# Kernel tuning notes

Hardware: AMD Instinct MI355X
Metric: run time of the kernel (lower is better)

Reference implementation:

```python
import jax, jax.numpy as jnp
import numpy as np

L = 2        # num_layers
D = 512      # d_model
H = 8        # heads
C = 512      # GAT per-head out channels (= d_model, concat=False -> mean over heads)
B, S, E = 4, 512, 4096
NEG = jnp.float32(-1e9)


def setup_inputs() -> dict:
    key = jax.random.key(0)
    ks = jax.random.split(key, 20)
    sc = 0.02  # weight init scale
    inp = {
        'x': jax.random.normal(ks[0], (B, S, D), jnp.float32),
        'Wq': jax.random.normal(ks[1], (L, D, D), jnp.float32) * sc,
        'bq': jnp.zeros((L, D), jnp.float32),
        'Wk': jax.random.normal(ks[2], (L, D, D), jnp.float32) * sc,
        'bk': jnp.zeros((L, D), jnp.float32),
        'Wv': jax.random.normal(ks[3], (L, D, D), jnp.float32) * sc,
        'bv': jnp.zeros((L, D), jnp.float32),
        'Wo': jax.random.normal(ks[4], (L, D, D), jnp.float32) * sc,
        'bo': jnp.zeros((L, D), jnp.float32),
        'gatW': jax.random.normal(ks[5], (L, D, H * C), jnp.float32) * sc,
        'att_src': jax.random.normal(ks[6], (L, H, C), jnp.float32) * sc,
        'att_dst': jax.random.normal(ks[7], (L, H, C), jnp.float32) * sc,
        'gat_bias': jnp.zeros((L, C), jnp.float32),
        'ln_g': jnp.ones((L, D), jnp.float32),
        'ln_b': jnp.zeros((L, D), jnp.float32),
        'input_len': jax.random.randint(ks[8], (B,), S // 2, S + 1, jnp.int32),
        'edges': jax.random.randint(ks[9], (B, 2, E), 0, S // 2, jnp.int32),
        'edge_num': jax.random.randint(ks[10], (B,), E // 2, E + 1, jnp.int32),
    }
    return inp


def layer_norm(x, g, b, eps=1e-5):
    m = x.mean(-1, keepdims=True)
    v = ((x - m) ** 2).mean(-1, keepdims=True)
    return (x - m) * jax.lax.rsqrt(v + eps) * g + b


def mha(x, pad_mask, Wq, bq, Wk, bk, Wv, bv, Wo, bo):
    # pad_mask: [B,S] True where padded (masked out)
    b, s, d = x.shape
    dh = d // H
    q = (x @ Wq + bq).reshape(b, s, H, dh)
    k = (x @ Wk + bk).reshape(b, s, H, dh)
    v = (x @ Wv + bv).reshape(b, s, H, dh)
    scores = jnp.einsum('bqhd,bkhd->bhqk', q, k) / jnp.float32(np.sqrt(dh))
    scores = jnp.where(pad_mask[:, None, None, :], NEG, scores)
    a = jax.nn.softmax(scores, axis=-1)
    o = jnp.einsum('bhqk,bkhd->bqhd', a, v).reshape(b, s, d)
    return o @ Wo + bo


def gat_single(x, edge_index, edge_mask, node_mask, W, a_src_w, a_dst_w, bias):
    # x: [S,D]; edge_index: [2,E]; GATConv(d_model,d_model,heads,concat=False)
    s = x.shape[0]
    h = (x @ W).reshape(s, H, C)
    a_src_n = (h * a_src_w).sum(-1)  # [S,H]
    a_dst_n = (h * a_dst_w).sum(-1)  # [S,H]
    # add self loops (PyG default) for valid nodes
    ar = jnp.arange(s, dtype=edge_index.dtype)
    src = jnp.concatenate([edge_index[0], ar])
    dst = jnp.concatenate([edge_index[1], ar])
    em = jnp.concatenate([edge_mask, node_mask])  # [E+S]
    alpha = jax.nn.leaky_relu(a_src_n[src] + a_dst_n[dst], 0.2)  # [E+S,H]
    alpha = jnp.where(em[:, None], alpha, NEG)
    amax = jax.ops.segment_max(alpha, dst, num_segments=s)  # [S,H]
    ex = jnp.exp(alpha - amax[dst]) * em[:, None].astype(alpha.dtype)
    denom = jax.ops.segment_sum(ex, dst, num_segments=s)
    coef = ex / (denom[dst] + 1e-16)
    msg = h[src] * coef[:, :, None]  # [E+S,H,C]
    out = jax.ops.segment_sum(msg, dst, num_segments=s)  # [S,H,C]
    return out.mean(axis=1) + bias  # concat=False -> mean over heads


def reference(x, Wq, bq, Wk, bk, Wv, bv, Wo, bo, gatW, att_src, att_dst,
              gat_bias, ln_g, ln_b, input_len, edges, edge_num):
    b, s, d = x.shape
    node_mask = jnp.arange(s)[None, :] < input_len[:, None]      # [B,S]
    edge_mask = jnp.arange(edges.shape[-1])[None, :] < edge_num[:, None]  # [B,E]
    pad_mask = ~node_mask
    out = x
    layer_outputs = []
    gat_b = jax.vmap(gat_single, in_axes=(0, 0, 0, 0, None, None, None, None))
    for i in range(L):
        out = mha(out, pad_mask, Wq[i], bq[i], Wk[i], bk[i], Wv[i], bv[i], Wo[i], bo[i])
        g = gat_b(out, edges, edge_mask, node_mask,
                  gatW[i], att_src[i], att_dst[i], gat_bias[i])
        y = jax.nn.relu(layer_norm(g, ln_g[i], ln_b[i])) + out
        out = jnp.where(node_mask[:, :, None], y, out)
        layer_outputs.append(out)
    return jnp.stack(layer_outputs)  # [L,B,S,D]
```

## Files before the change

kernel.cpp:

```cpp
#include <hip/hip_runtime.h>
#include <cstddef>

#define DMODEL 512
#define HEADS  8
#define DH     64
#define CCH    512
#define BATCH  4
#define SEQ    512
#define NEDGE  4096
#define NLAYER 2
#define HC     (HEADS*CCH)

typedef unsigned short bf16_t;
typedef __attribute__((ext_vector_type(8))) short short8;
typedef __attribute__((ext_vector_type(4))) float floatx4;

__device__ __forceinline__ bf16_t f2bf(float f){
  unsigned u = __float_as_uint(f);
  unsigned r = (u + 0x7FFFu + ((u>>16)&1u)) >> 16;
  return (bf16_t)r;
}
__device__ __forceinline__ float bf2f(bf16_t u){ return __uint_as_float(((unsigned)u)<<16); }

__global__ void k_zero(int* __restrict__ p, int n){
  int i = blockIdx.x*256 + threadIdx.x;
  if (i < n) p[i] = 0;
}

__global__ void k_f2b(const float* __restrict__ in, bf16_t* __restrict__ out, int n4){
  int i = blockIdx.x*256 + threadIdx.x;
  if (i < n4){
    float4 v = ((const float4*)in)[i];
    ushort4 o;
    o.x=f2bf(v.x); o.y=f2bf(v.y); o.z=f2bf(v.z); o.w=f2bf(v.w);
    ((ushort4*)out)[i]=o;
  }
}

struct WtJob { const float* W[10]; bf16_t* WT[10]; };
__global__ __launch_bounds__(256) void k_wt_all(WtJob j){
  __shared__ float T[32][65];
  int t = blockIdx.x, k0 = blockIdx.y*32;
  int wsel, n0, N;
  if (t < 64){ wsel = t>>3; n0 = (t&7)*64; N = 512; }
  else { int t2 = t-64; wsel = 8 + (t2>>6); n0 = (t2&63)*64; N = 4096; }
  const float* W = j.W[wsel];
  bf16_t* WT = j.WT[wsel];
  const int K = 512;
  int tid = threadIdx.x;
  int lk = tid>>3, ln = (tid&7)*8;
  const float* src = W + (size_t)(k0+lk)*N + n0 + ln;
  float4 v0 = *(const float4*)src;
  float4 v1 = *(const float4*)(src+4);
  T[lk][ln+0]=v0.x; T[lk][ln+1]=v0.y; T[lk][ln+2]=v0.z; T[lk][ln+3]=v0.w;
  T[lk][ln+4]=v1.x; T[lk][ln+5]=v1.y; T[lk][ln+6]=v1.z; T[lk][ln+7]=v1.w;
  __syncthreads();
  int wn = tid>>2, wk = (tid&3)*8;
  ushort4 o0, o1;
  o0.x=f2bf(T[wk+0][wn]); o0.y=f2bf(T[wk+1][wn]); o0.z=f2bf(T[wk+2][wn]); o0.w=f2bf(T[wk+3][wn]);
  o1.x=f2bf(T[wk+4][wn]); o1.y=f2bf(T[wk+5][wn]); o1.z=f2bf(T[wk+6][wn]); o1.w=f2bf(T[wk+7][wn]);
  bf16_t* dst = WT + (size_t)(n0+wn)*K + k0 + wk;
  *(ushort4*)dst = o0;
  *(ushort4*)(dst+4) = o1;
}

struct GemmB {
  const bf16_t* W; const float* bias; float* C; bf16_t* Cb;
  const float* att_s; const float* att_d; float* asrc; float* adst;
};
struct GemmB3 { GemmB g[3]; };

__global__ __launch_bounds__(256) void k_gemm_mfma(const bf16_t* __restrict__ A, GemmB3 p,
                                                   int N, int K){
  const GemmB& g = p.g[blockIdx.z];
  const bf16_t* Wt  = g.W;
  const float* bias = g.bias;
  float* C          = g.C;
  bf16_t* Cb        = g.Cb;
  __shared__ __align__(16) bf16_t As[2][64*72];
  __shared__ __align__(16) bf16_t Bs[2][64*72];
  int bm = blockIdx.x*64, bn = blockIdx.y*64;
  int tid = threadIdx.x;
  int wave = tid>>6, lane = tid&63;
  int wy = wave>>1, wx = wave&1;
  int quad = lane>>4, l16 = lane&15;
  floatx4 acc[2][2];
  #pragma unroll
  for (int i=0;i<2;i++)
    #pragma unroll
    for (int j=0;j<2;j++) acc[i][j] = (floatx4){0.f,0.f,0.f,0.f};
  int sr = tid>>2;
  int sc = (tid&3)<<4;
  const bf16_t* Aptr = A  + (size_t)(bm+sr)*K + sc;
  const bf16_t* Bptr = Wt + (size_t)(bn+sr)*K + sc;
  uint4 a0, a1, b0, b1;
  a0 = *(const uint4*)(Aptr);     a1 = *(const uint4*)(Aptr + 8);
  b0 = *(const uint4*)(Bptr);     b1 = *(const uint4*)(Bptr + 8);
  *(uint4*)(As[0] + sr*72 + sc)     = a0;
  *(uint4*)(As[0] + sr*72 + sc + 8) = a1;
  *(uint4*)(Bs[0] + sr*72 + sc)     = b0;
  *(uint4*)(Bs[0] + sr*72 + sc + 8) = b1;
  const int nk = K>>6;
  for (int k=0; k<nk; k++){
    __syncthreads();
    if (k+1 < nk){
      int ko = (k+1)<<6;
      a0 = *(const uint4*)(Aptr + ko);     a1 = *(const uint4*)(Aptr + ko + 8);
      b0 = *(const uint4*)(Bptr + ko);     b1 = *(const uint4*)(Bptr + ko + 8);
    }
    const bf16_t* Ab = As[k&1];
    const bf16_t* Bb = Bs[k&1];
    short8 af[2][2], bfr[2][2];
    #pragma unroll
    for (int i=0;i<2;i++){
      af[0][i] = *(const short8*)(Ab + (wy*32+i*16+l16)*72 + quad*8);
      af[1][i] = *(const short8*)(Ab + (wy*32+i*16+l16)*72 + 32 + quad*8);
    }
    #pragma unroll
    for (int j=0;j<2;j++){
      bfr[0][j] = *(const short8*)(Bb + (wx*32+j*16+l16)*72 + quad*8);
      bfr[1][j] = *(const short8*)(Bb + (wx*32+j*16+l16)*72 + 32 + quad*8);
    }
    #pragma unroll
    for (int i=0;i<2;i++)
      #pragma unroll
      for (int j=0;j<2;j++){
        acc[i][j] = __builtin_amdgcn_mfma_f32_16x16x32_bf16(af[0][i], bfr[0][j], acc[i][j], 0,0,0);
        acc[i][j] = __builtin_amdgcn_mfma_f32_16x16x32_bf16(af[1][i], bfr[1][j], acc[i][j], 0,0,0);
      }
    if (k+1 < nk){
      bf16_t* Aw = As[(k+1)&1];
      bf16_t* Bw = Bs[(k+1)&1];
      *(uint4*)(Aw + sr*72 + sc)     = a0;
      *(uint4*)(Aw + sr*72 + sc + 8) = a1;
      *(uint4*)(Bw + sr*72 + sc)     = b0;
      *(uint4*)(Bw + sr*72 + sc + 8) = b1;
    }
  }
  #pragma unroll
  for (int i=0;i<2;i++){
    int row = bm + wy*32 + i*16 + quad*4;
    #pragma unroll
    for (int j=0;j<2;j++){
      int col = bn + wx*32 + j*16 + l16;
      float bi = bias ? bias[col] : 0.f;
      #pragma unroll
      for (int r=0;r<4;r++){
        float vvv = acc[i][j][r] + bi;
        if (C)  C[(size_t)(row+r)*N + col] = vvv;
        if (Cb) Cb[(size_t)(row+r)*N + col] = f2bf(vvv);
      }
    }
  }
  if (g.asrc){
    int colbase = bn + wx*32;
    int hidx = colbase >> 9;
    float aw_s[2], aw_d[2];
    #pragma unroll
    for (int j=0;j<2;j++){
      int col = colbase + j*16 + l16;
      aw_s[j] = g.att_s[col];
      aw_d[j] = g.att_d[col];
    }
    #pragma unroll
    for (int i=0;i<2;i++){
      #pragma unroll
      for (int r=0;r<4;r++){
        float ps=0.f, pd=0.f;
        #pragma unroll
        for (int j=0;j<2;j++){ ps += acc[i][j][r]*aw_s[j]; pd += acc[i][j][r]*aw_d[j]; }
        #pragma unroll
        for (int m2=1;m2<16;m2<<=1){ ps += __shfl_xor(ps,m2); pd += __shfl_xor(pd,m2); }
        if (l16==0){
          int row = bm + wy*32 + i*16 + quad*4 + r;
          atomicAdd(&g.asrc[row*HEADS + hidx], ps);
          atomicAdd(&g.adst[row*HEADS + hidx], pd);
        }
      }
    }
  }
}

__global__ __launch_bounds__(256) void k_attn_flash(const bf16_t* __restrict__ q,
    const bf16_t* __restrict__ k, const bf16_t* __restrict__ v,
    const int* __restrict__ input_len, bf16_t* __restrict__ o){
  __shared__ __align__(16) bf16_t Kt[64*72];
  __shared__ __align__(16) bf16_t Vt[64*72];
  __shared__ __align__(16) bf16_t Pt[4][16*72];
  int q0 = blockIdx.x*64;
  int h  = blockIdx.y, b = blockIdx.z;
  int len = input_len[b];
  int tid = threadIdx.x;
  int w = tid>>6, lane = tid&63;
  int quad = lane>>4, l16 = lane&15;
  const bf16_t* qrow = q + ((size_t)(b*SEQ + q0 + w*16 + l16))*DMODEL + h*DH;
  short8 qa0 = *(const short8*)(qrow + quad*8);
  short8 qa1 = *(const short8*)(qrow + quad*8 + 32);
  int kr = tid>>2, kc = (tid&3)<<4;
  int vr = lane,   vc = w<<4;
  const bf16_t* kbase = k + ((size_t)(b*SEQ))*DMODEL + h*DH;
  const bf16_t* vbase = v + ((size_t)(b*SEQ))*DMODEL + h*DH;
  floatx4 oacc[4];
  #pragma unroll
  for (int dt=0;dt<4;dt++) oacc[dt] = (floatx4){0.f,0.f,0.f,0.f};
  float mrun[4], lrun[4];
  #pragma unroll
  for (int r=0;r<4;r++){ mrun[r]=-1e30f; lrun[r]=0.f; }
  for (int kt=0; kt<SEQ; kt+=64){
    if (kt >= len) break;
    uint4 kv0 = *(const uint4*)(kbase + (size_t)(kt+kr)*DMODEL + kc);
    uint4 kv1 = *(const uint4*)(kbase + (size_t)(kt+kr)*DMODEL + kc + 8);
    uint4 vv0 = *(const uint4*)(vbase + (size_t)(kt+vr)*DMODEL + vc);
    uint4 vv1 = *(const uint4*)(vbase + (size_t)(kt+vr)*DMODEL + vc + 8);
    __syncthreads();
    *(uint4*)(Kt + kr*72 + kc)     = kv0;
    *(uint4*)(Kt + kr*72 + kc + 8) = kv1;
    const ushort* vp0 = (const ushort*)&vv0;
    const ushort* vp1 = (const ushort*)&vv1;
    #pragma unroll
    for (int i2=0;i2<8;i2++) Vt[(vc+i2)*72 + vr]   = vp0[i2];
    #pragma unroll
    for (int i2=0;i2<8;i2++) Vt[(vc+8+i2)*72 + vr] = vp1[i2];
    __syncthreads();
    floatx4 sacc[4];
    #pragma unroll
    for (int nt=0;nt<4;nt++){
      sacc[nt] = (floatx4){0.f,0.f,0.f,0.f};
      short8 kb0 = *(const short8*)(Kt + (nt*16+l16)*72 + quad*8);
      short8 kb1 = *(const short8*)(Kt + (nt*16+l16)*72 + quad*8 + 32);
      sacc[nt] = __builtin_amdgcn_mfma_f32_16x16x32_bf16(qa0, kb0, sacc[nt], 0,0,0);
      sacc[nt] = __builtin_amdgcn_mfma_f32_16x16x32_bf16(qa1, kb1, sacc[nt], 0,0,0);
    }
    #pragma unroll
    for (int nt=0;nt<4;nt++){
      bool valid = (kt + nt*16 + l16) < len;
      #pragma unroll
      for (int r=0;r<4;r++){
        float sv = sacc[nt][r]*0.125f;
        sacc[nt][r] = valid ? sv : -1e30f;
      }
    }
    float alpha[4];
    #pragma unroll
    for (int r=0;r<4;r++){
      float mx = fmaxf(fmaxf(sacc[0][r],sacc[1][r]), fmaxf(sacc[2][r],sacc[3][r]));
      #pragma unroll
      for (int off=1; off<16; off<<=1) mx = fmaxf(mx, __shfl_xor(mx, off));
      float mn = fmaxf(mrun[r], mx);
      alpha[r] = __expf(mrun[r]-mn);
      mrun[r] = mn;
      float rs = 0.f;
      #pragma unroll
      for (int nt=0;nt<4;nt++){
        float pp = __expf(sacc[nt][r]-mn);
        sacc[nt][r] = pp; rs += pp;
      }
      #pragma unroll
      for (int off=1; off<16; off<<=1) rs += __shfl_xor(rs, off);
      lrun[r] = lrun[r]*alpha[r] + rs;
    }
    #pragma unroll
    for (int dt=0;dt<4;dt++)
      #pragma unroll
      for (int r=0;r<4;r++) oacc[dt][r] *= alpha[r];
    bf16_t* pw = Pt[w];
    #pragma unroll
    for (int nt=0;nt<4;nt++)
      #pragma unroll
      for (int r=0;r<4;r++) pw[(quad*4+r)*72 + nt*16 + l16] = f2bf(sacc[nt][r]);
    short8 pa0 = *(const short8*)(pw + l16*72 + quad*8);
    short8 pa1 = *(const short8*)(pw + l16*72 + quad*8 + 32);
    #pragma unroll
    for (int dt=0;dt<4;dt++){
      short8 vb0 = *(const short8*)(Vt + (dt*16+l16)*72 + quad*8);
      short8 vb1 = *(const short8*)(Vt + (dt*16+l16)*72 + quad*8 + 32);
      oacc[dt] = __builtin_amdgcn_mfma_f32_16x16x32_bf16(pa0, vb0, oacc[dt], 0,0,0);
      oacc[dt] = __builtin_amdgcn_mfma_f32_16x16x32_bf16(pa1, vb1, oacc[dt], 0,0,0);
    }
  }
  bf16_t* obase = o + ((size_t)(b*SEQ + q0 + w*16 + quad*4))*DMODEL + h*DH;
  #pragma unroll
  for (int r=0;r<4;r++){
    float invl = 1.f/lrun[r];
    #pragma unroll
    for (int dt=0;dt<4;dt++)
      obase[(size_t)r*DMODEL + dt*16 + l16] = f2bf(oacc[dt][r]*invl);
  }
}

__global__ void k_count(const int* __restrict__ edges, const int* __restrict__ edge_num, int* __restrict__ cnt){
  int b = blockIdx.y;
  int e = blockIdx.x*256 + threadIdx.x;
  if (e >= NEDGE || e >= edge_num[b]) return;
  int dst = edges[(size_t)b*2*NEDGE + NEDGE + e];
  atomicAdd(&cnt[b*SEQ + dst], 1);
}
__global__ void k_prefix(const int* __restrict__ cnt, int* __restrict__ offs, int* __restrict__ cursor){
  if (threadIdx.x==0){
    int b = blockIdx.x, acc=0;
    for (int s=0;s<SEQ;s++){ offs[b*SEQ+s]=acc; cursor[b*SEQ+s]=acc; acc+=cnt[b*SEQ+s]; }
  }
}
__global__ void k_fill(const int* __restrict__ edges, const int* __restrict__ edge_num,
                       int* __restrict__ cursor, int* __restrict__ elist){
  int b = blockIdx.y;
  int e = blockIdx.x*256 + threadIdx.x;
  if (e >= NEDGE || e >= edge_num[b]) return;
  int dst = edges[(size_t)b*2*NEDGE + NEDGE + e];
  int pos = atomicAdd(&cursor[b*SEQ + dst], 1);
  elist[(size_t)b*NEDGE + pos] = e;
}

__global__ __launch_bounds__(256) void k_gat_agg(const bf16_t* __restrict__ hbuf,
    const float* __restrict__ asrc, const float* __restrict__ adst,
    const int* __restrict__ offs, const int* __restrict__ cnt, const int* __restrict__ elist,
    const int* __restrict__ edges, const int* __restrict__ input_len,
    const float* __restrict__ gat_bias, float* __restrict__ gout){
  int s = blockIdx.x, b = blockIdx.y;
  if (s >= input_len[b]) return;
  __shared__ float amax_s[8], den_s[8], adl[8];
  __shared__ float cf[32][8];
  __shared__ int   cs[32];
  int tid = threadIdx.x;
  int n = cnt[b*SEQ+s];
  const int* el = elist + (size_t)b*NEDGE + offs[b*SEQ+s];
  const int* srcrow = edges + (size_t)b*2*NEDGE;
  if (tid < 8) adl[tid] = adst[(b*SEQ+s)*HEADS + tid];
  __syncthreads();
  if (tid < 64){
    float mx[8];
    #pragma unroll
    for (int h2=0;h2<8;h2++) mx[h2] = -1e30f;
    for (int j = tid; j <= n; j += 64){
      int src = (j==n) ? s : srcrow[el[j]];
      const float* ap = asrc + (size_t)(b*SEQ+src)*HEADS;
      #pragma unroll
      for (int h2=0;h2<8;h2++){
        float a = ap[h2] + adl[h2];
        a = (a>0.f)? a : 0.2f*a;
        mx[h2] = fmaxf(mx[h2], a);
      }
    }
    #pragma unroll
    for (int h2=0;h2<8;h2++){
      float vmx = mx[h2];
      #pragma unroll
      for (int off=32; off; off>>=1) vmx = fmaxf(vmx, __shfl_xor(vmx,off,64));
      mx[h2]=vmx;
    }
    float sm[8];
    #pragma unroll
    for (int h2=0;h2<8;h2++) sm[h2]=0.f;
    for (int j = tid; j <= n; j += 64){
      int src = (j==n) ? s : srcrow[el[j]];
      const float* ap = asrc + (size_t)(b*SEQ+src)*HEADS;
      #pragma unroll
      for (int h2=0;h2<8;h2++){
        float a = ap[h2] + adl[h2];
        a = (a>0.f)? a : 0.2f*a;
        sm[h2] += __expf(a - mx[h2]);
      }
    }
    #pragma unroll
    for (int h2=0;h2<8;h2++){
      float vs = sm[h2];
      #pragma unroll
      for (int off=32; off; off>>=1) vs += __shfl_xor(vs,off,64);
      if (tid==0){ amax_s[h2]=mx[h2]; den_s[h2]=vs; }
    }
  }
  __syncthreads();
  float acc0=0.f, acc1=0.f;
  int c0 = tid*2;
  for (int j0=0; j0 <= n; j0 += 32){
    int jm = min(32, n+1-j0);
    if (tid < jm*8){
      int jj = j0 + (tid>>3), h2 = tid&7;
      int src = (jj==n) ? s : srcrow[el[jj]];
      if (h2==0) cs[tid>>3] = src;
      float a = asrc[(size_t)(b*SEQ+src)*HEADS + h2] + adl[h2];
      a = (a>0.f)? a : 0.2f*a;
      cf[tid>>3][h2] = __expf(a - amax_s[h2]) / (den_s[h2] + 1e-16f);
    }
    __syncthreads();
    for (int jj=0; jj<jm; ++jj){
      int src = cs[jj];
      const bf16_t* hrow = hbuf + ((size_t)(b*SEQ+src))*HC;
      #pragma unroll
      for (int h2=0;h2<8;h2++){
        float wgt = cf[jj][h2];
        ushort2 hv = *(const ushort2*)(hrow + h2*CCH + c0);
        acc0 += wgt * bf2f(hv.x);
        acc1 += wgt * bf2f(hv.y);
      }
    }
    __syncthreads();
  }
  size_t gbse = ((size_t)(b*SEQ+s))*CCH;
  float2 outv = { acc0*0.125f + gat_bias[c0], acc1*0.125f + gat_bias[c0+1] };
  *(float2*)(gout + gbse + c0) = outv;
}

__global__ __launch_bounds__(256) void k_combine(const float* __restrict__ gbuf, const float* __restrict__ xin,
    const float* __restrict__ lng, const float* __restrict__ lnb,
    const int* __restrict__ input_len, bf16_t* __restrict__ curb, float* __restrict__ outp){
  __shared__ float red[256];
  int s = blockIdx.x, b = blockIdx.y, tid = threadIdx.x;
  size_t row = ((size_t)(b*SEQ+s))*DMODEL;
  float x0 = xin[row+tid], x1 = xin[row+tid+256];
  float y0 = x0, y1 = x1;
  if (s < input_len[b]){
    float g0 = gbuf[row+tid], g1 = gbuf[row+tid+256];
    red[tid] = g0+g1;
    __syncthreads();
    for (int off=128; off; off>>=1){ if (tid<off) red[tid]+=red[tid+off]; __syncthreads(); }
    float mean = red[0]*(1.f/512.f);
    __syncthreads();
    float d0 = g0-mean, d1 = g1-mean;
    red[tid] = d0*d0 + d1*d1;
    __syncthreads();
    for (int off=128; off; off>>=1){ if (tid<off) red[tid]+=red[tid+off]; __syncthreads(); }
    float inv = rsqrtf(red[0]*(1.f/512.f) + 1e-5f);
    float t0 = d0*inv*lng[tid]     + lnb[tid];
    float t1 = d1*inv*lng[tid+256] + lnb[tid+256];
    y0 = fmaxf(t0,0.f) + x0;
    y1 = fmaxf(t1,0.f) + x1;
  }
  curb[row+tid]=f2bf(y0); curb[row+tid+256]=f2bf(y1);
  outp[row+tid]=y0; outp[row+tid+256]=y1;
}

extern "C" void kernel_launch(void* const* d_in, const int* in_sizes, int n_in,
                              void* d_out, int out_size, void* d_ws, size_t ws_size,
                              hipStream_t stream){
  (void)in_sizes; (void)n_in; (void)out_size; (void)ws_size;
  const float* x       = (const float*)d_in[0];
  const float* Wq      = (const float*)d_in[1];
  const float* bq      = (const float*)d_in[2];
  const float* Wk      = (const float*)d_in[3];
  const float* bk      = (const float*)d_in[4];
  const float* Wv      = (const float*)d_in[5];
  const float* bv      = (const float*)d_in[6];
  const float* Wo      = (const float*)d_in[7];
  const float* bo      = (const float*)d_in[8];
  const float* gatW    = (const float*)d_in[9];
  const float* att_src = (const float*)d_in[10];
  const float* att_dst = (const float*)d_in[11];
  const float* gat_bias= (const float*)d_in[12];
  const float* ln_g    = (const float*)d_in[13];
  const float* ln_b    = (const float*)d_in[14];
  const int* input_len  = (const int*)d_in[15];
  const int* edges      = (const int*)d_in[16];
  const int* edge_num   = (const int*)d_in[17];
  float* outp = (float*)d_out;

  char* w = (char*)d_ws;
  size_t off = 0;
  auto alloc = [&](size_t bytes)->char*{ char* p = w + off; off += (bytes + 255) & ~(size_t)255; return p; };
  const size_t BSD = (size_t)BATCH*SEQ*DMODEL;
  const size_t BSH = (size_t)BATCH*SEQ*HEADS;
  float* mha  = (float*)alloc(BSD*4);
  bf16_t* hb  = (bf16_t*)alloc((size_t)BATCH*SEQ*HC*2);
  float* gb   = (float*)alloc(BSD*4);
  float* attn_nodes = (float*)alloc(2*BSH*4);
  float* asrc = attn_nodes;
  float* adst = attn_nodes + BSH;
  int* cnt    = (int*)alloc(BATCH*SEQ*4);
  int* offs   = (int*)alloc(BATCH*SEQ*4);
  int* cursor = (int*)alloc(BATCH*SEQ*4);
  int* elist  = (int*)alloc((size_t)BATCH*NEDGE*4);
  bf16_t* xbf  = (bf16_t*)alloc(BSD*2);
  bf16_t* curb = (bf16_t*)alloc(BSD*2);
  bf16_t* qbf  = (bf16_t*)alloc(BSD*2);
  bf16_t* kbf  = (bf16_t*)alloc(BSD*2);
  bf16_t* vbf  = (bf16_t*)alloc(BSD*2);
  bf16_t* obf  = (bf16_t*)alloc(BSD*2);
  bf16_t* abf  = (bf16_t*)alloc(BSD*2);
  bf16_t* wqt  = (bf16_t*)alloc((size_t)NLAYER*DMODEL*DMODEL*2);
  bf16_t* wkt  = (bf16_t*)alloc((size_t)NLAYER*DMODEL*DMODEL*2);
  bf16_t* wvt  = (bf16_t*)alloc((size_t)NLAYER*DMODEL*DMODEL*2);
  bf16_t* wot  = (bf16_t*)alloc((size_t)NLAYER*DMODEL*DMODEL*2);
  bf16_t* gwt  = (bf16_t*)alloc((size_t)NLAYER*DMODEL*HC*2);

  k_zero<<<dim3((BATCH*SEQ+255)/256),256,0,stream>>>(cnt, BATCH*SEQ);
  k_count<<<dim3(NEDGE/256, BATCH),256,0,stream>>>(edges, edge_num, cnt);
  k_prefix<<<dim3(BATCH),64,0,stream>>>(cnt, offs, cursor);
  k_fill<<<dim3(NEDGE/256, BATCH),256,0,stream>>>(edges, edge_num, cursor, elist);

  WtJob wj;
  for (int i=0;i<NLAYER;i++){
    size_t wo = (size_t)i*DMODEL*DMODEL;
    wj.W[i*4+0]=Wq+wo;  wj.WT[i*4+0]=wqt+wo;
    wj.W[i*4+1]=Wk+wo;  wj.WT[i*4+1]=wkt+wo;
    wj.W[i*4+2]=Wv+wo;  wj.WT[i*4+2]=wvt+wo;
    wj.W[i*4+3]=Wo+wo;  wj.WT[i*4+3]=wot+wo;
    size_t go = (size_t)i*DMODEL*HC;
    wj.W[8+i]=gatW+go;  wj.WT[8+i]=gwt+go;
  }
  k_wt_all<<<dim3(192, 16),256,0,stream>>>(wj);
  k_f2b<<<dim3((unsigned)(BSD/4/256)),256,0,stream>>>(x, xbf, (int)(BSD/4));

  const int M = BATCH*SEQ;
  for (int i=0;i<NLAYER;i++){
    size_t wo = (size_t)i*DMODEL*DMODEL;
    size_t bo2 = (size_t)i*DMODEL;
    const bf16_t* Ab = (i==0) ? xbf : curb;
    GemmB3 qkv;
    qkv.g[0] = { wqt+wo, bq+bo2, nullptr, qbf, nullptr, nullptr, nullptr, nullptr };
    qkv.g[1] = { wkt+wo, bk+bo2, nullptr, kbf, nullptr, nullptr, nullptr, nullptr };
    qkv.g[2] = { wvt+wo, bv+bo2, nullptr, vbf, nullptr, nullptr, nullptr, nullptr };
    k_gemm_mfma<<<dim3(M/64, DMODEL/64, 3),256,0,stream>>>(Ab, qkv, DMODEL, DMODEL);
    k_attn_flash<<<dim3(SEQ/64, HEADS, BATCH),256,0,stream>>>(qbf, kbf, vbf, input_len, obf);
    GemmB3 og;
    og.g[0] = { wot+wo, bo+bo2, mha, abf, nullptr, nullptr, nullptr, nullptr };
    og.g[1] = og.g[0]; og.g[2] = og.g[0];
    k_gemm_mfma<<<dim3(M/64, DMODEL/64, 1),256,0,stream>>>(obf, og, DMODEL, DMODEL);
    k_zero<<<dim3((unsigned)((2*BSH+255)/256)),256,0,stream>>>((int*)attn_nodes, (int)(2*BSH));
    GemmB3 gg;
    gg.g[0] = { gwt + (size_t)i*DMODEL*HC, nullptr, nullptr, hb,
                att_src + (size_t)i*HC, att_dst + (size_t)i*HC, asrc, adst };
    gg.g[1] = gg.g[0]; gg.g[2] = gg.g[0];
    k_gemm_mfma<<<dim3(M/64, HC/64, 1),256,0,stream>>>(abf, gg, HC, DMODEL);
    k_gat_agg<<<dim3(SEQ, BATCH),256,0,stream>>>(hb, asrc, adst, offs, cnt, elist, edges, input_len, gat_bias + (size_t)i*CCH, gb);
    k_combine<<<dim3(SEQ, BATCH),256,0,stream>>>(gb, mha, ln_g+bo2, ln_b+bo2, input_len, curb, outp + (size_t)i*BSD);
  }
}
```

Baseline: 320.3 us.

## Fuse edge CSR build into one kernel and GAT aggregation with layernorm combine

Replaces the four edge-preprocessing kernels (zero, count, prefix, fill) with one per-batch block that builds the CSR in shared memory and also zeroes both layers' attention-logit buffers. That removes the per-layer zero launch. It also fuses the GAT aggregation with the layernorm/relu/residual combine, so the fp32 GAT output no longer round-trips through global memory. This saves launches and memory traffic, at the cost of a serial single-block edge build and a heavier fused kernel.

```diff
diff --git a/kernel.cpp b/kernel.cpp
--- a/kernel.cpp
+++ b/kernel.cpp
@@ -22,11 +22,6 @@
 }
 __device__ __forceinline__ float bf2f(bf16_t u){ return __uint_as_float(((unsigned)u)<<16); }
 
-__global__ void k_zero(int* __restrict__ p, int n){
-  int i = blockIdx.x*256 + threadIdx.x;
-  if (i < n) p[i] = 0;
-}
-
 __global__ void k_f2b(const float* __restrict__ in, bf16_t* __restrict__ out, int n4){
   int i = blockIdx.x*256 + threadIdx.x;
   if (i < n4){
@@ -34,6 +29,39 @@
     ushort4 o;
     o.x=f2bf(v.x); o.y=f2bf(v.y); o.z=f2bf(v.z); o.w=f2bf(v.w);
     ((ushort4*)out)[i]=o;
+  }
+}
+
+__global__ __launch_bounds__(256) void k_edges(const int* __restrict__ edges,
+    const int* __restrict__ edge_num, int* __restrict__ cnt, int* __restrict__ offs,
+    int* __restrict__ elist, float* __restrict__ attn_nodes, int an_total){
+  __shared__ int cnt_l[SEQ];
+  __shared__ int off_l[SEQ];
+  __shared__ int cur_l[SEQ];
+  int b = blockIdx.x, tid = threadIdx.x;
+  int chunk = an_total / BATCH;
+  for (int i = tid; i < chunk; i += 256) attn_nodes[b*chunk + i] = 0.f;
+  for (int s = tid; s < SEQ; s += 256) cnt_l[s] = 0;
+  __syncthreads();
+  int ne = edge_num[b];
+  const int* dstrow = edges + (size_t)b*2*NEDGE + NEDGE;
+  for (int e = tid; e < ne; e += 256) atomicAdd(&cnt_l[dstrow[e]], 1);
+  __syncthreads();
+  if (tid == 0){
+    int acc = 0;
+    for (int s = 0; s < SEQ; s++){ off_l[s] = acc; acc += cnt_l[s]; }
+  }
+  __syncthreads();
+  for (int s = tid; s < SEQ; s += 256) cur_l[s] = off_l[s];
+  __syncthreads();
+  for (int e = tid; e < ne; e += 256){
+    int dst = dstrow[e];
+    int pos = atomicAdd(&cur_l[dst], 1);
+    elist[(size_t)b*NEDGE + pos] = e;
+  }
+  for (int s = tid; s < SEQ; s += 256){
+    cnt[b*SEQ + s]  = cnt_l[s];
+    offs[b*SEQ + s] = off_l[s];
   }
 }
 
@@ -288,40 +316,28 @@
   }
 }
 
-__global__ void k_count(const int* __restrict__ edges, const int* __restrict__ edge_num, int* __restrict__ cnt){
-  int b = blockIdx.y;
-  int e = blockIdx.x*256 + threadIdx.x;
-  if (e >= NEDGE || e >= edge_num[b]) return;
-  int dst = edges[(size_t)b*2*NEDGE + NEDGE + e];
-  atomicAdd(&cnt[b*SEQ + dst], 1);
-}
-__global__ void k_prefix(const int* __restrict__ cnt, int* __restrict__ offs, int* __restrict__ cursor){
-  if (threadIdx.x==0){
-    int b = blockIdx.x, acc=0;
-    for (int s=0;s<SEQ;s++){ offs[b*SEQ+s]=acc; cursor[b*SEQ+s]=acc; acc+=cnt[b*SEQ+s]; }
-  }
-}
-__global__ void k_fill(const int* __restrict__ edges, const int* __restrict__ edge_num,
-                       int* __restrict__ cursor, int* __restrict__ elist){
-  int b = blockIdx.y;
-  int e = blockIdx.x*256 + threadIdx.x;
-  if (e >= NEDGE || e >= edge_num[b]) return;
-  int dst = edges[(size_t)b*2*NEDGE + NEDGE + e];
-  int pos = atomicAdd(&cursor[b*SEQ + dst], 1);
-  elist[(size_t)b*NEDGE + pos] = e;
-}
-
-__global__ __launch_bounds__(256) void k_gat_agg(const bf16_t* __restrict__ hbuf,
+__global__ __launch_bounds__(256) void k_gat_ln(const bf16_t* __restrict__ hbuf,
     const float* __restrict__ asrc, const float* __restrict__ adst,
     const int* __restrict__ offs, const int* __restrict__ cnt, const int* __restrict__ elist,
     const int* __restrict__ edges, const int* __restrict__ input_len,
-    const float* __restrict__ gat_bias, float* __restrict__ gout){
+    const float* __restrict__ gat_bias, const float* __restrict__ mha,
+    const float* __restrict__ lng, const float* __restrict__ lnb,
+    bf16_t* __restrict__ curb, float* __restrict__ outp){
   int s = blockIdx.x, b = blockIdx.y;
-  if (s >= input_len[b]) return;
+  int tid = threadIdx.x;
+  size_t row = ((size_t)(b*SEQ+s))*DMODEL;
+  int c0 = tid*2;
+  float2 xv = *(const float2*)(mha + row + c0);
+  if (s >= input_len[b]){
+    curb[row+c0]   = f2bf(xv.x);
+    curb[row+c0+1] = f2bf(xv.y);
+    *(float2*)(outp + row + c0) = xv;
+    return;
+  }
   __shared__ float amax_s[8], den_s[8], adl[8];
   __shared__ float cf[32][8];
   __shared__ int   cs[32];
-  int tid = threadIdx.x;
+  __shared__ float red[256];
   int n = cnt[b*SEQ+s];
   const int* el = elist + (size_t)b*NEDGE + offs[b*SEQ+s];
   const int* srcrow = edges + (size_t)b*2*NEDGE;
@@ -371,7 +387,6 @@
   }
   __syncthreads();
   float acc0=0.f, acc1=0.f;
-  int c0 = tid*2;
   for (int j0=0; j0 <= n; j0 += 32){
     int jm = min(32, n+1-j0);
     if (tid < jm*8){
@@ -396,38 +411,26 @@
     }
     __syncthreads();
   }
-  size_t gbse = ((size_t)(b*SEQ+s))*CCH;
-  float2 outv = { acc0*0.125f + gat_bias[c0], acc1*0.125f + gat_bias[c0+1] };
-  *(float2*)(gout + gbse + c0) = outv;
-}
-
-__global__ __launch_bounds__(256) void k_combine(const float* __restrict__ gbuf, const float* __restrict__ xin,
-    const float* __restrict__ lng, const float* __restrict__ lnb,
-    const int* __restrict__ input_len, bf16_t* __restrict__ curb, float* __restrict__ outp){
-  __shared__ float red[256];
-  int s = blockIdx.x, b = blockIdx.y, tid = threadIdx.x;
-  size_t row = ((size_t)(b*SEQ+s))*DMODEL;
-  float x0 = xin[row+tid], x1 = xin[row+tid+256];
-  float y0 = x0, y1 = x1;
-  if (s < input_len[b]){
-    float g0 = gbuf[row+tid], g1 = gbuf[row+tid+256];
-    red[tid] = g0+g1;
-    __syncthreads();
-    for (int off=128; off; off>>=1){ if (tid<off) red[tid]+=red[tid+off]; __syncthreads(); }
-    float mean = red[0]*(1.f/512.f);
-    __syncthreads();
-    float d0 = g0-mean, d1 = g1-mean;
-    red[tid] = d0*d0 + d1*d1;
-    __syncthreads();
-    for (int off=128; off; off>>=1){ if (tid<off) red[tid]+=red[tid+off]; __syncthreads(); }
-    float inv = rsqrtf(red[0]*(1.f/512.f) + 1e-5f);
-    float t0 = d0*inv*lng[tid]     + lnb[tid];
-    float t1 = d1*inv*lng[tid+256] + lnb[tid+256];
-    y0 = fmaxf(t0,0.f) + x0;
-    y1 = fmaxf(t1,0.f) + x1;
-  }
-  curb[row+tid]=f2bf(y0); curb[row+tid+256]=f2bf(y1);
-  outp[row+tid]=y0; outp[row+tid+256]=y1;
+  float g0 = acc0*0.125f + gat_bias[c0];
+  float g1 = acc1*0.125f + gat_bias[c0+1];
+  red[tid] = g0+g1;
+  __syncthreads();
+  for (int off=128; off; off>>=1){ if (tid<off) red[tid]+=red[tid+off]; __syncthreads(); }
+  float mean = red[0]*(1.f/512.f);
+  __syncthreads();
+  float d0 = g0-mean, d1 = g1-mean;
+  red[tid] = d0*d0 + d1*d1;
+  __syncthreads();
+  for (int off=128; off; off>>=1){ if (tid<off) red[tid]+=red[tid+off]; __syncthreads(); }
+  float inv = rsqrtf(red[0]*(1.f/512.f) + 1e-5f);
+  float t0 = d0*inv*lng[c0]   + lnb[c0];
+  float t1 = d1*inv*lng[c0+1] + lnb[c0+1];
+  float y0 = fmaxf(t0,0.f) + xv.x;
+  float y1 = fmaxf(t1,0.f) + xv.y;
+  curb[row+c0]   = f2bf(y0);
+  curb[row+c0+1] = f2bf(y1);
+  float2 outv = { y0, y1 };
+  *(float2*)(outp + row + c0) = outv;
 }
 
 extern "C" void kernel_launch(void* const* d_in, const int* in_sizes, int n_in,
@@ -461,13 +464,9 @@
   const size_t BSH = (size_t)BATCH*SEQ*HEADS;
   float* mha  = (float*)alloc(BSD*4);
   bf16_t* hb  = (bf16_t*)alloc((size_t)BATCH*SEQ*HC*2);
-  float* gb   = (float*)alloc(BSD*4);
-  float* attn_nodes = (float*)alloc(2*BSH*4);
-  float* asrc = attn_nodes;
-  float* adst = attn_nodes + BSH;
+  float* attn_nodes = (float*)alloc((size_t)NLAYER*2*BSH*4);
   int* cnt    = (int*)alloc(BATCH*SEQ*4);
   int* offs   = (int*)alloc(BATCH*SEQ*4);
-  int* cursor = (int*)alloc(BATCH*SEQ*4);
   int* elist  = (int*)alloc((size_t)BATCH*NEDGE*4);
   bf16_t* xbf  = (bf16_t*)alloc(BSD*2);
   bf16_t* curb = (bf16_t*)alloc(BSD*2);
@@ -482,11 +481,8 @@
   bf16_t* wot  = (bf16_t*)alloc((size_t)NLAYER*DMODEL*DMODEL*2);
   bf16_t* gwt  = (bf16_t*)alloc((size_t)NLAYER*DMODEL*HC*2);
 
-  k_zero<<<dim3((BATCH*SEQ+255)/256),256,0,stream>>>(cnt, BATCH*SEQ);
-  k_count<<<dim3(NEDGE/256, BATCH),256,0,stream>>>(edges, edge_num, cnt);
-  k_prefix<<<dim3(BATCH),64,0,stream>>>(cnt, offs, cursor);
-  k_fill<<<dim3(NEDGE/256, BATCH),256,0,stream>>>(edges, edge_num, cursor, elist);
-
+  k_edges<<<dim3(BATCH),256,0,stream>>>(edges, edge_num, cnt, offs, elist,
+                                        attn_nodes, (int)(NLAYER*2*BSH));
   WtJob wj;
   for (int i=0;i<NLAYER;i++){
     size_t wo = (size_t)i*DMODEL*DMODEL;
@@ -504,6 +500,8 @@
   for (int i=0;i<NLAYER;i++){
     size_t wo = (size_t)i*DMODEL*DMODEL;
     size_t bo2 = (size_t)i*DMODEL;
+    float* asrc = attn_nodes + (size_t)i*2*BSH;
+    float* adst = asrc + BSH;
     const bf16_t* Ab = (i==0) ? xbf : curb;
     GemmB3 qkv;
     qkv.g[0] = { wqt+wo, bq+bo2, nullptr, qbf, nullptr, nullptr, nullptr, nullptr };
@@ -515,13 +513,13 @@
     og.g[0] = { wot+wo, bo+bo2, mha, abf, nullptr, nullptr, nullptr, nullptr };
     og.g[1] = og.g[0]; og.g[2] = og.g[0];
     k_gemm_mfma<<<dim3(M/64, DMODEL/64, 1),256,0,stream>>>(obf, og, DMODEL, DMODEL);
-    k_zero<<<dim3((unsigned)((2*BSH+255)/256)),256,0,stream>>>((int*)attn_nodes, (int)(2*BSH));
     GemmB3 gg;
     gg.g[0] = { gwt + (size_t)i*DMODEL*HC, nullptr, nullptr, hb,
                 att_src + (size_t)i*HC, att_dst + (size_t)i*HC, asrc, adst };
     gg.g[1] = gg.g[0]; gg.g[2] = gg.g[0];
     k_gemm_mfma<<<dim3(M/64, HC/64, 1),256,0,stream>>>(abf, gg, HC, DMODEL);
-    k_gat_agg<<<dim3(SEQ, BATCH),256,0,stream>>>(hb, asrc, adst, offs, cnt, elist, edges, input_len, gat_bias + (size_t)i*CCH, gb);
-    k_combine<<<dim3(SEQ, BATCH),256,0,stream>>>(gb, mha, ln_g+bo2, ln_b+bo2, input_len, curb, outp + (size_t)i*BSD);
-  }
-}
+    k_gat_ln<<<dim3(SEQ, BATCH),256,0,stream>>>(hb, asrc, adst, offs, cnt, elist, edges,
+        input_len, gat_bias + (size_t)i*CCH, mha, ln_g+bo2, ln_b+bo2,
+        curb, outp + (size_t)i*BSD);
+  }
+}
```

Result: faster. 310.7 us (-3.0%).
